# Performance work log

Measured on AMD Instinct MI355X. Metric: run time of the kernel, lower is better.

## Reference

```python
import jax, jax.numpy as jnp
import numpy as np

B, N, K, H = 8, 4096, 32, 256
LN_EPS = 1e-5


def setup_inputs() -> dict:
    key = jax.random.key(0)
    k1, k2, k3, k4, k5 = jax.random.split(key, 5)
    h = jax.random.normal(k1, (B, N, H), dtype=jnp.float32)
    nbr_idx = jax.random.randint(k2, (B, N, K), 0, N, dtype=jnp.int64)
    nbr_w = jax.random.uniform(k3, (B, N, K), dtype=jnp.float32)
    # Linear weights stored torch-style as [out, in]; y = x @ W.T
    W_self = jax.random.normal(k4, (H, H), dtype=jnp.float32) / np.sqrt(H)
    W_neigh = jax.random.normal(k5, (H, H), dtype=jnp.float32) / np.sqrt(H)
    ln_gamma = jnp.ones((H,), dtype=jnp.float32)
    ln_beta = jnp.zeros((H,), dtype=jnp.float32)
    return {"h": h, "nbr_idx": nbr_idx, "nbr_w": nbr_w, "W_self": W_self,
            "W_neigh": W_neigh, "ln_gamma": ln_gamma, "ln_beta": ln_beta}


def _layer_norm(x, gamma, beta):
    mu = jnp.mean(x, axis=-1, keepdims=True)
    var = jnp.mean(jnp.square(x - mu), axis=-1, keepdims=True)
    return (x - mu) * jax.lax.rsqrt(var + LN_EPS) * gamma + beta


def reference(h, nbr_idx, nbr_w, W_self, W_neigh, ln_gamma, ln_beta):
    b, n, hd = h.shape
    k = nbr_idx.shape[2]
    # gather neighbor features: [B, N, k, H]
    flat_idx = nbr_idx.reshape(b, n * k)
    h_nbr = jnp.take_along_axis(h, flat_idx[:, :, None], axis=1).reshape(b, n, k, hd)
    # weighted aggregate over neighbors
    h_agg = jnp.einsum('bnk,bnkh->bnh', nbr_w, h_nbr)
    # dual linear + exact (erf) GELU, matching torch nn.GELU default
    out = jax.nn.gelu(h @ W_self.T + h_agg @ W_neigh.T, approximate=False)
    # dropout is identity in eval mode
    return _layer_norm(out, ln_gamma, ln_beta)
```

## Files before the change

### kernel.cpp

```cpp
#include <hip/hip_runtime.h>
#include <hip/hip_bf16.h>
#include <math.h>
#include <stdint.h>

constexpr int Nn = 4096, Kk = 32, Hh = 256;
constexpr int Mm = 8 * Nn;

typedef float  f32x4 __attribute__((ext_vector_type(4)));
typedef short  s16x8 __attribute__((ext_vector_type(8)));

static __device__ __forceinline__ ushort f2bf(float f) {
  uint32_t u = __float_as_uint(f);
  u += 0x7FFF + ((u >> 16) & 1);
  return (ushort)(u >> 16);
}
static __device__ __forceinline__ float bf2f(ushort s) {
  return __uint_as_float(((uint32_t)s) << 16);
}
static __device__ __forceinline__ void gl_lds16(const ushort* g, ushort* l) {
  __builtin_amdgcn_global_load_lds(
      (const __attribute__((address_space(1))) void*)g,
      (__attribute__((address_space(3))) void*)l, 16, 0, 0);
}
static __device__ __forceinline__ float gelu_t(float x) {
  float u = x * x;
  float y = x * (1.5957691216f + 0.0713548162726f * u);
  float t = __expf(y);
  return x - x * __builtin_amdgcn_rcpf(t + 1.0f);
}

__global__ void detect_idx(const int* __restrict__ p, int* __restrict__ flag) {
  int t = threadIdx.x;
  unsigned long long b = __ballot(p[2 * t + 1] != 0);
  if (t == 0) *flag = (b != 0ULL) ? 1 : 0;
}

__global__ __launch_bounds__(256) void prep_w(const float* __restrict__ Ws,
                                              const float* __restrict__ Wn,
                                              ushort* __restrict__ Wc) {
  int i = blockIdx.x * 256 + threadIdx.x;
  int j  = i >> 6;
  int k4 = i & 63;
  const float* src = (j < 256) ? (Ws + (size_t)j * 256 + k4 * 4)
                               : (Wn + (size_t)(j - 256) * 256 + k4 * 4);
  float4 v = *reinterpret_cast<const float4*>(src);
  ushort4 o = { f2bf(v.x), f2bf(v.y), f2bf(v.z), f2bf(v.w) };
  reinterpret_cast<ushort4*>(Wc)[i] = o;
}

__global__ __launch_bounds__(512, 4) void gemm1(const float* __restrict__ h,
                                                const ushort* __restrict__ Wc,
                                                ushort* __restrict__ hs,
                                                ushort* __restrict__ hn) {
  __shared__ ushort lA[2][64 * 64];
  __shared__ ushort lB[2][256 * 64];
  const int tid = threadIdx.x, wid = tid >> 6, lane = tid & 63;
  const int wr = wid >> 1, wc = wid & 1;

  const int blk = blockIdx.x;
  const int b = blk & 7, t = blk >> 3;
  const int nblk = t & 1, mblk = t >> 1;
  const int m0 = b * Nn + mblk * 64;
  const ushort* Wbase = Wc + (size_t)nblk * 256 * 256;

  f32x4 acc[8];
  #pragma unroll
  for (int j = 0; j < 8; ++j) acc[j] = f32x4{0.f, 0.f, 0.f, 0.f};

  float4 a0, a1;
  const int ar = tid >> 3, as = tid & 7;
  auto aload = [&](int kt) {
    const float* src = h + (size_t)(m0 + ar) * 256 + kt * 64 + as * 8;
    a0 = *reinterpret_cast<const float4*>(src);
    a1 = *reinterpret_cast<const float4*>(src + 4);
  };
  auto awrite = [&](int buf) {
    s16x8 u = { (short)f2bf(a0.x), (short)f2bf(a0.y), (short)f2bf(a0.z),
                (short)f2bf(a0.w), (short)f2bf(a1.x), (short)f2bf(a1.y),
                (short)f2bf(a1.z), (short)f2bf(a1.w) };
    *reinterpret_cast<s16x8*>(&lA[buf][ar * 64 + ((as ^ (ar & 7)) << 3)]) = u;
  };
  auto bstage = [&](int buf, int kt) {
    #pragma unroll
    for (int c = 0; c < 4; ++c) {
      int ch = wid + c * 8;
      int r = ch * 8 + (lane >> 3);
      int s = (lane & 7) ^ (r & 7);
      gl_lds16(Wbase + (size_t)r * 256 + kt * 64 + s * 8, &lB[buf][ch * 512]);
    }
  };

  aload(0);
  bstage(0, 0);
  awrite(0);
  __syncthreads();

  int buf = 0;
  for (int kt = 0; kt < 4; ++kt) {
    if (kt < 3) { aload(kt + 1); bstage(buf ^ 1, kt + 1); }
    #pragma unroll
    for (int kk = 0; kk < 2; ++kk) {
      const int ks = kk * 4 + (lane >> 4);
      const int ra = wr * 16 + (lane & 15);
      s16x8 af = *reinterpret_cast<const s16x8*>(
          &lA[buf][ra * 64 + ((ks ^ (ra & 7)) << 3)]);
      s16x8 bfr[8];
      #pragma unroll
      for (int nj = 0; nj < 8; ++nj) {
        int rb = wc * 128 + nj * 16 + (lane & 15);
        bfr[nj] = *reinterpret_cast<const s16x8*>(
            &lB[buf][rb * 64 + ((ks ^ (rb & 7)) << 3)]);
      }
      #pragma unroll
      for (int nj = 0; nj < 8; ++nj)
        acc[nj] = __builtin_amdgcn_mfma_f32_16x16x32_bf16(af, bfr[nj],
                                                          acc[nj], 0, 0, 0);
    }
    if (kt < 3) awrite(buf ^ 1);
    __syncthreads();
    buf ^= 1;
  }

  ushort* dst = (nblk == 0) ? hs : hn;
  #pragma unroll
  for (int nj = 0; nj < 8; ++nj)
    #pragma unroll
    for (int jj = 0; jj < 4; ++jj) {
      int row = wr * 16 + (lane >> 4) * 4 + jj;
      int col = wc * 128 + nj * 16 + (lane & 15);
      dst[(size_t)(m0 + row) * 256 + col] = f2bf(acc[nj][jj]);
    }
}

__global__ __launch_bounds__(256, 4) void k2(const ushort* __restrict__ hs,
                                             const ushort* __restrict__ hn,
                                             const void* __restrict__ idx,
                                             const float* __restrict__ w,
                                             const float* __restrict__ gamma,
                                             const float* __restrict__ beta,
                                             float* __restrict__ out,
                                             const int* __restrict__ flag) {
  const int wv = threadIdx.x >> 6, lane = threadIdx.x & 63;
  const int b = blockIdx.x & 7;
  const int m = b * Nn + (blockIdx.x >> 3) * 4 + wv;
  const int is32 = *flag;

  size_t kbase = (size_t)m * Kk + (lane & 31);
  int myi = is32 ? ((const int*)idx)[kbase] : (int)((const long long*)idx)[kbase];
  float myw = w[kbase];

  const ushort4* hs4 = reinterpret_cast<const ushort4*>(hs);
  const ushort4* hn4 = reinterpret_cast<const ushort4*>(hn) + (size_t)b * Nn * 64;

  float4 acc;
  {
    ushort4 v = hs4[(size_t)m * 64 + lane];
    acc.x = bf2f(v.x); acc.y = bf2f(v.y); acc.z = bf2f(v.z); acc.w = bf2f(v.w);
  }
  #pragma unroll
  for (int k = 0; k < Kk; ++k) {
    int r    = __shfl(myi, k, 64);
    float wt = __shfl(myw, k, 64);
    ushort4 v = hn4[(size_t)r * 64 + lane];
    acc.x += wt * bf2f(v.x);
    acc.y += wt * bf2f(v.y);
    acc.z += wt * bf2f(v.z);
    acc.w += wt * bf2f(v.w);
  }

  float g0 = gelu_t(acc.x), g1 = gelu_t(acc.y), g2 = gelu_t(acc.z), g3 = gelu_t(acc.w);
  float sv = g0 + g1 + g2 + g3;
  float qv = g0 * g0 + g1 * g1 + g2 * g2 + g3 * g3;
  #pragma unroll
  for (int msk = 32; msk >= 1; msk >>= 1) {
    sv += __shfl_xor(sv, msk, 64);
    qv += __shfl_xor(qv, msk, 64);
  }
  float mean = sv * (1.0f / 256.0f);
  float var  = qv * (1.0f / 256.0f) - mean * mean;
  float inv  = rsqrtf(var + 1e-5f);

  float4 gm = reinterpret_cast<const float4*>(gamma)[lane];
  float4 bt = reinterpret_cast<const float4*>(beta)[lane];
  float4 o;
  o.x = (g0 - mean) * inv * gm.x + bt.x;
  o.y = (g1 - mean) * inv * gm.y + bt.y;
  o.z = (g2 - mean) * inv * gm.z + bt.z;
  o.w = (g3 - mean) * inv * gm.w + bt.w;
  reinterpret_cast<float4*>(out)[(size_t)m * 64 + lane] = o;
}

extern "C" void kernel_launch(void* const* d_in, const int* in_sizes, int n_in,
                              void* d_out, int out_size, void* d_ws, size_t ws_size,
                              hipStream_t stream) {
  const float* h     = (const float*)d_in[0];
  const void*  idx   = d_in[1];
  const float* w     = (const float*)d_in[2];
  const float* Ws    = (const float*)d_in[3];
  const float* Wn    = (const float*)d_in[4];
  const float* gamma = (const float*)d_in[5];
  const float* beta  = (const float*)d_in[6];
  float* out = (float*)d_out;

  ushort* hs = (ushort*)d_ws;
  ushort* hn = hs + (size_t)Mm * Hh;
  ushort* Wc = hn + (size_t)Mm * Hh;
  int* flag  = (int*)(Wc + 512 * 256);

  detect_idx<<<1, 64, 0, stream>>>((const int*)idx, flag);
  prep_w<<<128, 256, 0, stream>>>(Ws, Wn, Wc);
  gemm1<<<1024, 512, 0, stream>>>(h, Wc, hs, hn);
  k2<<<Mm / 4, 256, 0, stream>>>(hs, hn, idx, w, gamma, beta, out, flag);
}
```

Before: 66.84 us.

## Process two rows per wave with 16-byte gathers and software-prefetched neighbors

The gather/aggregate kernel now maps each half-wave to one output row, so each lane loads 8 bf16 values (16 bytes) per neighbor instead of 4. Neighbor loads are software-pipelined four at a time, with split accumulators to break dependency chains. Blocks grow to 512 threads covering 16 rows. This aims to raise memory-level parallelism and cut load-instruction count in the latency-bound gather, at the cost of more registers per thread.

```diff
diff --git a/kernel.cpp b/kernel.cpp
--- a/kernel.cpp
+++ b/kernel.cpp
@@ -132,7 +132,7 @@
     }
 }
 
-__global__ __launch_bounds__(256, 4) void k2(const ushort* __restrict__ hs,
+__global__ __launch_bounds__(512, 4) void k2(const ushort* __restrict__ hs,
                                              const ushort* __restrict__ hn,
                                              const void* __restrict__ idx,
                                              const float* __restrict__ w,
@@ -140,39 +140,58 @@
                                              const float* __restrict__ beta,
                                              float* __restrict__ out,
                                              const int* __restrict__ flag) {
-  const int wv = threadIdx.x >> 6, lane = threadIdx.x & 63;
+  const int tid = threadIdx.x, wv = tid >> 6, lane = tid & 63;
+  const int hw = lane >> 5, l5 = lane & 31;
   const int b = blockIdx.x & 7;
-  const int m = b * Nn + (blockIdx.x >> 3) * 4 + wv;
+  const int m = b * Nn + (blockIdx.x >> 3) * 16 + wv * 2 + hw;
   const int is32 = *flag;
 
-  size_t kbase = (size_t)m * Kk + (lane & 31);
-  int myi = is32 ? ((const int*)idx)[kbase] : (int)((const long long*)idx)[kbase];
-  float myw = w[kbase];
-
-  const ushort4* hs4 = reinterpret_cast<const ushort4*>(hs);
-  const ushort4* hn4 = reinterpret_cast<const ushort4*>(hn) + (size_t)b * Nn * 64;
-
-  float4 acc;
-  {
-    ushort4 v = hs4[(size_t)m * 64 + lane];
-    acc.x = bf2f(v.x); acc.y = bf2f(v.y); acc.z = bf2f(v.z); acc.w = bf2f(v.w);
-  }
-  #pragma unroll
-  for (int k = 0; k < Kk; ++k) {
-    int r    = __shfl(myi, k, 64);
-    float wt = __shfl(myw, k, 64);
-    ushort4 v = hn4[(size_t)r * 64 + lane];
-    acc.x += wt * bf2f(v.x);
-    acc.y += wt * bf2f(v.y);
-    acc.z += wt * bf2f(v.z);
-    acc.w += wt * bf2f(v.w);
-  }
-
-  float g0 = gelu_t(acc.x), g1 = gelu_t(acc.y), g2 = gelu_t(acc.z), g3 = gelu_t(acc.w);
-  float sv = g0 + g1 + g2 + g3;
-  float qv = g0 * g0 + g1 * g1 + g2 * g2 + g3 * g3;
-  #pragma unroll
-  for (int msk = 32; msk >= 1; msk >>= 1) {
+  size_t kb = (size_t)m * Kk + l5;
+  int   myi = is32 ? ((const int*)idx)[kb] : (int)((const long long*)idx)[kb];
+  float myw = w[kb];
+
+  const ushort* hnb = hn + (size_t)b * Nn * Hh;
+
+  auto ld = [&](int k) -> s16x8 {
+    int r = __shfl(myi, k, 32);
+    return *reinterpret_cast<const s16x8*>(hnb + ((size_t)r << 8) + (l5 << 3));
+  };
+
+  f32x4 aA0{0,0,0,0}, aA1{0,0,0,0}, aB0{0,0,0,0}, aB1{0,0,0,0};
+  s16x8 p0 = ld(0), p1 = ld(1), p2 = ld(2), p3 = ld(3);
+
+  #pragma unroll
+  for (int k = 0; k < 32; k += 4) {
+    float w0 = __shfl(myw, k, 32),     w1 = __shfl(myw, k + 1, 32);
+    float w2 = __shfl(myw, k + 2, 32), w3 = __shfl(myw, k + 3, 32);
+    s16x8 q0 = p0, q1 = p1, q2 = p2, q3 = p3;
+    if (k + 4 < 32) { p0 = ld(k + 4); p1 = ld(k + 5); p2 = ld(k + 6); p3 = ld(k + 7); }
+    #pragma unroll
+    for (int j = 0; j < 4; ++j) {
+      aA0[j] += w0 * bf2f((ushort)q0[j]);
+      aA1[j] += w0 * bf2f((ushort)q0[j + 4]);
+      aA0[j] += w1 * bf2f((ushort)q1[j]);
+      aA1[j] += w1 * bf2f((ushort)q1[j + 4]);
+      aB0[j] += w2 * bf2f((ushort)q2[j]);
+      aB1[j] += w2 * bf2f((ushort)q2[j + 4]);
+      aB0[j] += w3 * bf2f((ushort)q3[j]);
+      aB1[j] += w3 * bf2f((ushort)q3[j + 4]);
+    }
+  }
+
+  s16x8 hv = *reinterpret_cast<const s16x8*>(hs + (size_t)m * Hh + l5 * 8);
+  float g[8];
+  #pragma unroll
+  for (int j = 0; j < 4; ++j) {
+    g[j]     = gelu_t(aA0[j] + aB0[j] + bf2f((ushort)hv[j]));
+    g[j + 4] = gelu_t(aA1[j] + aB1[j] + bf2f((ushort)hv[j + 4]));
+  }
+
+  float sv = 0.f, qv = 0.f;
+  #pragma unroll
+  for (int j = 0; j < 8; ++j) { sv += g[j]; qv += g[j] * g[j]; }
+  #pragma unroll
+  for (int msk = 16; msk >= 1; msk >>= 1) {
     sv += __shfl_xor(sv, msk, 64);
     qv += __shfl_xor(qv, msk, 64);
   }
@@ -180,14 +199,22 @@
   float var  = qv * (1.0f / 256.0f) - mean * mean;
   float inv  = rsqrtf(var + 1e-5f);
 
-  float4 gm = reinterpret_cast<const float4*>(gamma)[lane];
-  float4 bt = reinterpret_cast<const float4*>(beta)[lane];
-  float4 o;
-  o.x = (g0 - mean) * inv * gm.x + bt.x;
-  o.y = (g1 - mean) * inv * gm.y + bt.y;
-  o.z = (g2 - mean) * inv * gm.z + bt.z;
-  o.w = (g3 - mean) * inv * gm.w + bt.w;
-  reinterpret_cast<float4*>(out)[(size_t)m * 64 + lane] = o;
+  float4 gm0 = reinterpret_cast<const float4*>(gamma)[l5 * 2];
+  float4 gm1 = reinterpret_cast<const float4*>(gamma)[l5 * 2 + 1];
+  float4 bt0 = reinterpret_cast<const float4*>(beta)[l5 * 2];
+  float4 bt1 = reinterpret_cast<const float4*>(beta)[l5 * 2 + 1];
+  float4 o0, o1;
+  o0.x = (g[0] - mean) * inv * gm0.x + bt0.x;
+  o0.y = (g[1] - mean) * inv * gm0.y + bt0.y;
+  o0.z = (g[2] - mean) * inv * gm0.z + bt0.z;
+  o0.w = (g[3] - mean) * inv * gm0.w + bt0.w;
+  o1.x = (g[4] - mean) * inv * gm1.x + bt1.x;
+  o1.y = (g[5] - mean) * inv * gm1.y + bt1.y;
+  o1.z = (g[6] - mean) * inv * gm1.z + bt1.z;
+  o1.w = (g[7] - mean) * inv * gm1.w + bt1.w;
+  float4* op = reinterpret_cast<float4*>(out + (size_t)m * Hh + l5 * 8);
+  op[0] = o0;
+  op[1] = o1;
 }
 
 extern "C" void kernel_launch(void* const* d_in, const int* in_sizes, int n_in,
@@ -210,5 +237,5 @@
   detect_idx<<<1, 64, 0, stream>>>((const int*)idx, flag);
   prep_w<<<128, 256, 0, stream>>>(Ws, Wn, Wc);
   gemm1<<<1024, 512, 0, stream>>>(h, Wc, hs, hn);
-  k2<<<Mm / 4, 256, 0, stream>>>(hs, hn, idx, w, gamma, beta, out, flag);
-}
+  k2<<<2048, 512, 0, stream>>>(hs, hn, idx, w, gamma, beta, out, flag);
+}
```

Result: faster. 60.45 us (-9.6%).
